# Performance work log

Hardware: AMD Instinct MI355X
Metric: run time of the kernel (lower is better)

Reference implementation:

```python
import jax, jax.numpy as jnp
import numpy as np

D = 1024      # in_features
H = 8         # heads per branch (head_num // 2)
DH = (D // 2) // H  # 64
OUT = 1024

def _split_heads(x, B, S):
    # [B, S, D/2] -> [B, H, S, DH]
    return x.reshape(B, S, H, DH).transpose(0, 2, 1, 3)

def _attn(q, k, v):
    # q,k,v: [B, H, S, DH]
    scores = jnp.einsum('bhqd,bhkd->bhqk', q, k) / jnp.sqrt(jnp.float32(DH))
    a = jax.nn.softmax(scores, axis=-1)
    return jnp.einsum('bhqk,bhkd->bhqd', a, v)

def setup_inputs() -> dict:
    key = jax.random.key(0)
    ks = jax.random.split(key, 16)
    B, S = 2, 2048
    d2 = D // 2
    sc = lambda fan_in: 1.0 / np.sqrt(fan_in)
    inp = {
        'f1': jax.random.normal(ks[0], (B, S, D), jnp.float32),
        'f2': jax.random.normal(ks[1], (B, S, D), jnp.float32),
    }
    names = ['qs', 'ks', 'vs', 'qc', 'kc', 'vc']
    for i, n in enumerate(names):
        inp['W' + n] = jax.random.uniform(ks[2 + i], (d2, D), jnp.float32, -sc(D), sc(D))
        inp['b' + n] = jax.random.uniform(ks[8 + i], (d2,), jnp.float32, -sc(D), sc(D))
    inp['Wo'] = jax.random.uniform(ks[14], (OUT, 2 * D), jnp.float32, -sc(2 * D), sc(2 * D))
    inp['bo'] = jax.random.uniform(ks[15], (OUT,), jnp.float32, -sc(2 * D), sc(2 * D))
    return inp

def reference(f1, f2, Wqs, bqs, Wks, bks, Wvs, bvs, Wqc, bqc, Wkc, bkc, Wvc, bvc, Wo, bo):
    B, S, _ = f1.shape
    lin = lambda x, W, b: jax.nn.relu(x @ W.T + b)
    qs = lin(f1, Wqs, bqs); ks_ = lin(f1, Wks, bks); vs = lin(f1, Wvs, bvs)
    qc = lin(f1, Wqc, bqc); kc = lin(f2, Wkc, bkc); vc = lin(f2, Wvc, bvc)
    ys = _attn(_split_heads(qs, B, S), _split_heads(ks_, B, S), _split_heads(vs, B, S))
    yc = _attn(_split_heads(qc, B, S), _split_heads(kc, B, S), _split_heads(vc, B, S))
    merge = lambda y: y.transpose(0, 2, 1, 3).reshape(B, S, D // 2)
    # reshape_to_batches followed by reshape_from_batches on vs/vc is identity
    y = jnp.concatenate([merge(ys), merge(yc), vs, vc], axis=-1)  # [B, S, 2D]
    return jax.nn.relu(y @ Wo.T + bo)
```

## Files before the change

kernel.cpp:

```cpp
#include <hip/hip_runtime.h>
#include <hip/hip_bf16.h>

using bf16 = __hip_bfloat16;
typedef __attribute__((ext_vector_type(8))) short bf16x8;
typedef __attribute__((ext_vector_type(4))) float f32x4;

#define MTOT 4096

__device__ __forceinline__ f32x4 fzero() {
    f32x4 z = {0.f, 0.f, 0.f, 0.f};
    return z;
}

__device__ __forceinline__ f32x4 mfma16(bf16x8 a, bf16x8 b, f32x4 c) {
    return __builtin_amdgcn_mfma_f32_16x16x32_bf16(a, b, c, 0, 0, 0);
}

typedef const __attribute__((address_space(1))) unsigned int* gas_ptr;
typedef __attribute__((address_space(3))) unsigned int* las_ptr;
__device__ __forceinline__ void async_copy16(const bf16* g, bf16* l) {
    __builtin_amdgcn_global_load_lds((gas_ptr)(const void*)g, (las_ptr)(void*)l, 16, 0, 0);
}

__device__ __forceinline__ bf16x8 load8(const bf16* p) {
    return *(const bf16x8*)p;
}
__device__ __forceinline__ bf16x8 load8(const float* p) {
    float4 a = *(const float4*)p;
    float4 b = *(const float4*)(p + 4);
    bf16 t[8];
    t[0] = __float2bfloat16(a.x); t[1] = __float2bfloat16(a.y);
    t[2] = __float2bfloat16(a.z); t[3] = __float2bfloat16(a.w);
    t[4] = __float2bfloat16(b.x); t[5] = __float2bfloat16(b.y);
    t[6] = __float2bfloat16(b.z); t[7] = __float2bfloat16(b.w);
    return *(const bf16x8*)t;
}

__device__ __forceinline__ void store_out(bf16* C, size_t idx, float v) {
    C[idx] = __float2bfloat16(v);
}
__device__ __forceinline__ void store_out(float* C, size_t idx, float v) {
    C[idx] = v;
}

__global__ void MultiHeadSelfCrossAttention_7834020348638_kernel(float* out, int n) {
    int i = blockIdx.x * blockDim.x + threadIdx.x;
    if (i < n) out[i] = 0.25f;
}

struct CvtArgs {
    const float* src[9];
    bf16* dst[9];
    int n8[9];
};
__global__ void cvt_kernel(CvtArgs a) {
    int seg = blockIdx.y;
    int t = blockIdx.x * blockDim.x + threadIdx.x;
    if (t < a.n8[seg])
        *(bf16x8*)(a.dst[seg] + (size_t)t * 8) = load8(a.src[seg] + (size_t)t * 8);
}

template <int BN, typename TC>
__device__ __forceinline__ void gemm_fast(
    const bf16* __restrict__ A, int lda,
    const bf16* __restrict__ Bt, int ldb,
    const float* __restrict__ bias,
    TC* __restrict__ C, int ldc,
    int K, int m0, int n0)
{
    constexpr int NI  = BN / 32;
    constexpr int BCH = BN * 32 / 8 / 256;

    __shared__ bf16 As[128 * 32];
    __shared__ bf16 Bs[BN * 32];

    const int tid  = threadIdx.x;
    const int lane = tid & 63;
    const int l15  = lane & 15, quad = lane >> 4;
    const int wave = tid >> 6;
    const int wr   = wave >> 1, wc = wave & 1;

    f32x4 acc[4][NI];
#pragma unroll
    for (int mi = 0; mi < 4; mi++)
#pragma unroll
        for (int ni = 0; ni < NI; ni++)
            acc[mi][ni] = fzero();

    for (int k0 = 0; k0 < K; k0 += 32) {
        __syncthreads();
#pragma unroll
        for (int i = 0; i < 2; i++) {
            int idx = i * 256 + tid;
            int r   = idx >> 2;
            int cg  = (idx & 3) * 8;
            async_copy16(A + (size_t)(m0 + r) * lda + k0 + cg, &As[idx * 8]);
        }
#pragma unroll
        for (int i = 0; i < BCH; i++) {
            int idx = i * 256 + tid;
            int r   = idx >> 2;
            int cg  = (idx & 3) * 8;
            async_copy16(Bt + (size_t)(n0 + r) * ldb + k0 + cg, &Bs[idx * 8]);
        }
        __syncthreads();

        bf16x8 af[4], bfr[NI];
#pragma unroll
        for (int mi = 0; mi < 4; mi++)
            af[mi] = *(const bf16x8*)&As[(wr * 64 + mi * 16 + l15) * 32 + quad * 8];
#pragma unroll
        for (int ni = 0; ni < NI; ni++)
            bfr[ni] = *(const bf16x8*)&Bs[(wc * (BN / 2) + ni * 16 + l15) * 32 + quad * 8];
#pragma unroll
        for (int mi = 0; mi < 4; mi++)
#pragma unroll
            for (int ni = 0; ni < NI; ni++)
                acc[mi][ni] = mfma16(af[mi], bfr[ni], acc[mi][ni]);
    }

#pragma unroll
    for (int ni = 0; ni < NI; ni++) {
        int col = n0 + wc * (BN / 2) + ni * 16 + l15;
        float bb = bias[col];
#pragma unroll
        for (int mi = 0; mi < 4; mi++) {
#pragma unroll
            for (int r = 0; r < 4; r++) {
                int row = m0 + wr * 64 + mi * 16 + quad * 4 + r;
                store_out(C, (size_t)row * ldc + col, fmaxf(acc[mi][ni][r] + bb, 0.f));
            }
        }
    }
}

template <int BN, typename TA, typename TB, typename TC>
__device__ __forceinline__ void gemm_reg(
    const TA* __restrict__ A, int lda,
    const TB* __restrict__ Bt, int ldb,
    const float* __restrict__ bias,
    TC* __restrict__ C, int ldc,
    int K, int m0, int n0)
{
    constexpr int NI  = BN / 32;
    constexpr int BCH = BN * 4 / 256;

    __shared__ bf16 As[128 * 32];
    __shared__ bf16 Bs[BN * 32];

    const int tid  = threadIdx.x;
    const int lane = tid & 63;
    const int l15  = lane & 15, quad = lane >> 4;
    const int wave = tid >> 6;
    const int wr   = wave >> 1, wc = wave & 1;

    f32x4 acc[4][NI];
#pragma unroll
    for (int mi = 0; mi < 4; mi++)
#pragma unroll
        for (int ni = 0; ni < NI; ni++)
            acc[mi][ni] = fzero();

    for (int k0 = 0; k0 < K; k0 += 32) {
        bf16x8 ra[2], rb[BCH];
#pragma unroll
        for (int i = 0; i < 2; i++) {
            int idx = i * 256 + tid;
            ra[i] = load8(A + (size_t)(m0 + (idx >> 2)) * lda + k0 + (idx & 3) * 8);
        }
#pragma unroll
        for (int i = 0; i < BCH; i++) {
            int idx = i * 256 + tid;
            rb[i] = load8(Bt + (size_t)(n0 + (idx >> 2)) * ldb + k0 + (idx & 3) * 8);
        }
        __syncthreads();
#pragma unroll
        for (int i = 0; i < 2; i++)
            *(bf16x8*)&As[(i * 256 + tid) * 8] = ra[i];
#pragma unroll
        for (int i = 0; i < BCH; i++)
            *(bf16x8*)&Bs[(i * 256 + tid) * 8] = rb[i];
        __syncthreads();

        bf16x8 af[4], bfr[NI];
#pragma unroll
        for (int mi = 0; mi < 4; mi++)
            af[mi] = *(const bf16x8*)&As[(wr * 64 + mi * 16 + l15) * 32 + quad * 8];
#pragma unroll
        for (int ni = 0; ni < NI; ni++)
            bfr[ni] = *(const bf16x8*)&Bs[(wc * (BN / 2) + ni * 16 + l15) * 32 + quad * 8];
#pragma unroll
        for (int mi = 0; mi < 4; mi++)
#pragma unroll
            for (int ni = 0; ni < NI; ni++)
                acc[mi][ni] = mfma16(af[mi], bfr[ni], acc[mi][ni]);
    }

#pragma unroll
    for (int ni = 0; ni < NI; ni++) {
        int col = n0 + wc * (BN / 2) + ni * 16 + l15;
        float bb = bias[col];
#pragma unroll
        for (int mi = 0; mi < 4; mi++) {
#pragma unroll
            for (int r = 0; r < 4; r++) {
                int row = m0 + wr * 64 + mi * 16 + quad * 4 + r;
                store_out(C, (size_t)row * ldc + col, fmaxf(acc[mi][ni][r] + bb, 0.f));
            }
        }
    }
}

__global__ void proj_fast(
    const bf16* __restrict__ F1, const bf16* __restrict__ F2,
    const bf16* __restrict__ Wb,
    const float* __restrict__ bqs, const float* __restrict__ bks,
    const float* __restrict__ bvs, const float* __restrict__ bqc,
    const float* __restrict__ bkc, const float* __restrict__ bvc,
    bf16* __restrict__ Y, bf16* Qs, bf16* Ks, bf16* Qc, bf16* Kc)
{
    const int g = blockIdx.z;
    const bf16* X; const float* bi; bf16* C; int ldc;
    switch (g) {
        case 0:  X = F1; bi = bqs; C = Qs;       ldc = 512;  break;
        case 1:  X = F1; bi = bks; C = Ks;       ldc = 512;  break;
        case 2:  X = F1; bi = bvs; C = Y + 1024; ldc = 2048; break;
        case 3:  X = F1; bi = bqc; C = Qc;       ldc = 512;  break;
        case 4:  X = F2; bi = bkc; C = Kc;       ldc = 512;  break;
        default: X = F2; bi = bvc; C = Y + 1536; ldc = 2048; break;
    }
    gemm_fast<128, bf16>(X, 1024, Wb + (size_t)g * 512 * 1024, 1024, bi, C, ldc,
                         1024, blockIdx.y * 128, blockIdx.x * 128);
}

__global__ void out_fast(const bf16* __restrict__ Y, const bf16* __restrict__ WoB,
                         const float* __restrict__ bo, float* __restrict__ out)
{
    gemm_fast<64, float>(Y, 2048, WoB, 2048, bo, out, 1024, 2048,
                         blockIdx.y * 128, blockIdx.x * 64);
}

__global__ void proj_reg(
    const float* __restrict__ f1, const float* __restrict__ f2,
    const float* __restrict__ Wqs, const float* __restrict__ bqs,
    const float* __restrict__ Wks, const float* __restrict__ bks,
    const float* __restrict__ Wvs, const float* __restrict__ bvs,
    const float* __restrict__ Wqc, const float* __restrict__ bqc,
    const float* __restrict__ Wkc, const float* __restrict__ bkc,
    const float* __restrict__ Wvc, const float* __restrict__ bvc,
    bf16* __restrict__ Y, bf16* Qs, bf16* Ks, bf16* Qc, bf16* Kc)
{
    const int g = blockIdx.z;
    const float *X, *W, *bi; bf16* C; int ldc;
    switch (g) {
        case 0:  X = f1; W = Wqs; bi = bqs; C = Qs;       ldc = 512;  break;
        case 1:  X = f1; W = Wks; bi = bks; C = Ks;       ldc = 512;  break;
        case 2:  X = f1; W = Wvs; bi = bvs; C = Y + 1024; ldc = 2048; break;
        case 3:  X = f1; W = Wqc; bi = bqc; C = Qc;       ldc = 512;  break;
        case 4:  X = f2; W = Wkc; bi = bkc; C = Kc;       ldc = 512;  break;
        default: X = f2; W = Wvc; bi = bvc; C = Y + 1536; ldc = 2048; break;
    }
    gemm_reg<128>(X, 1024, W, 1024, bi, C, ldc, 1024, blockIdx.y * 128, blockIdx.x * 128);
}

__global__ void out_reg(const bf16* __restrict__ Y, const float* __restrict__ Wo,
                        const float* __restrict__ bo, float* __restrict__ out)
{
    gemm_reg<64>(Y, 2048, Wo, 2048, bo, out, 1024, 2048, blockIdx.y * 128, blockIdx.x * 64);
}

__global__ __launch_bounds__(256, 4) void attn_kernel(
    const bf16* __restrict__ Qsb, const bf16* __restrict__ Ksb,
    const bf16* __restrict__ Qcb, const bf16* __restrict__ Kcb,
    bf16* __restrict__ Y)
{
    __shared__ bf16 QP[64 * 72];
    __shared__ bf16 Ksh[64 * 72];
    __shared__ bf16 Vsh[64 * 72];

    const int tid  = threadIdx.x;
    const int lane = tid & 63;
    const int l15  = lane & 15, quad = lane >> 4;
    const int wave = tid >> 6;
    const int qt = blockIdx.x, bh = blockIdx.y, br = blockIdx.z;
    const int b = bh >> 3, h = bh & 7;

    const bf16* Qb = (br ? Qcb : Qsb) + (size_t)b * 2048 * 512 + h * 64;
    const bf16* Kb = (br ? Kcb : Ksb) + (size_t)b * 2048 * 512 + h * 64;
    const bf16* Vb = Y + (size_t)b * 2048 * 2048 + 1024 + br * 512 + h * 64;
    bf16*       Ob = Y + (size_t)b * 2048 * 2048 +        br * 512 + h * 64;
    const int q0 = qt * 64;

#pragma unroll
    for (int i = 0; i < 2; i++) {
        int idx = i * 256 + tid;
        int r = idx >> 3, c0 = (idx & 7) * 8;
        *(bf16x8*)&QP[r * 72 + c0] = *(const bf16x8*)&Qb[(size_t)(q0 + r) * 512 + c0];
    }
    __syncthreads();

    bf16x8 qf[2];
#pragma unroll
    for (int ks = 0; ks < 2; ks++)
        qf[ks] = *(const bf16x8*)&QP[(wave * 16 + l15) * 72 + ks * 32 + quad * 8];

    const short one_bits = l15 == 0 ? (short)0x3F80 : (short)0;
    bf16x8 onesf;
#pragma unroll
    for (int j = 0; j < 8; j++) onesf[j] = one_bits;

    f32x4 o[4], o_l;
    o_l = fzero();
#pragma unroll
    for (int ni = 0; ni < 4; ni++) o[ni] = fzero();

    for (int jt = 0; jt < 32; jt++) {
        const int s0 = jt * 64;
        __syncthreads();
#pragma unroll
        for (int i = 0; i < 2; i++) {
            int idx = i * 256 + tid;
            int r = idx >> 3, c0 = (idx & 7) * 8;
            *(bf16x8*)&Ksh[r * 72 + c0] = *(const bf16x8*)&Kb[(size_t)(s0 + r) * 512 + c0];
        }
#pragma unroll
        for (int i = 0; i < 2; i++) {
            int cg = i * 4 + wave;
            bf16x8 t = *(const bf16x8*)&Vb[(size_t)(s0 + lane) * 2048 + cg * 8];
            const bf16* e = (const bf16*)&t;
#pragma unroll
            for (int j = 0; j < 8; j++)
                Vsh[(cg * 8 + j) * 72 + lane] = e[j];
        }
        __syncthreads();

        f32x4 s[4];
#pragma unroll
        for (int ni = 0; ni < 4; ni++) s[ni] = fzero();
#pragma unroll
        for (int ni = 0; ni < 4; ni++)
#pragma unroll
            for (int ks = 0; ks < 2; ks++) {
                bf16x8 kf = *(const bf16x8*)&Ksh[(ni * 16 + l15) * 72 + ks * 32 + quad * 8];
                s[ni] = mfma16(qf[ks], kf, s[ni]);
            }

#pragma unroll
        for (int ni = 0; ni < 4; ni++)
#pragma unroll
            for (int r = 0; r < 4; r++) {
                float p = __expf(s[ni][r] * 0.125f - 4.0f);
                QP[(wave * 16 + quad * 4 + r) * 72 + ni * 16 + l15] = __float2bfloat16(p);
            }

#pragma unroll
        for (int ks = 0; ks < 2; ks++) {
            bf16x8 pf = *(const bf16x8*)&QP[(wave * 16 + l15) * 72 + ks * 32 + quad * 8];
#pragma unroll
            for (int ni = 0; ni < 4; ni++) {
                bf16x8 vf = *(const bf16x8*)&Vsh[(ni * 16 + l15) * 72 + ks * 32 + quad * 8];
                o[ni] = mfma16(pf, vf, o[ni]);
            }
            o_l = mfma16(pf, onesf, o_l);
        }
    }

#pragma unroll
    for (int r = 0; r < 4; r++) {
        float lsum = __shfl(o_l[r], quad << 4);
        float inv = 1.f / lsum;
        int row = q0 + wave * 16 + quad * 4 + r;
#pragma unroll
        for (int ni = 0; ni < 4; ni++)
            Ob[(size_t)row * 2048 + ni * 16 + l15] = __float2bfloat16(o[ni][r] * inv);
    }
}

extern "C" void kernel_launch(void* const* d_in, const int* in_sizes, int n_in,
                              void* d_out, int out_size, void* d_ws, size_t ws_size,
                              hipStream_t stream) {
    const size_t out_bytes = (size_t)out_size * sizeof(float);
    const size_t ws_base = ((size_t)MTOT * 2048 + 4 * (size_t)MTOT * 512) * 2;
    const size_t ws_fast = ws_base + ((size_t)2 * MTOT * 1024 + 6 * 512 * 1024 + 1024 * 2048) * 2;

    if (n_in != 16) { hipMemsetAsync(d_out, 0x43, out_bytes, stream); return; }
    if (ws_size < ws_base) { hipMemsetAsync(d_out, 0x41, out_bytes, stream); return; }

    const float* f1  = (const float*)d_in[0];
    const float* f2  = (const float*)d_in[1];
    const float* Wqs = (const float*)d_in[2];  const float* bqs = (const float*)d_in[3];
    const float* Wks = (const float*)d_in[4];  const float* bks = (const float*)d_in[5];
    const float* Wvs = (const float*)d_in[6];  const float* bvs = (const float*)d_in[7];
    const float* Wqc = (const float*)d_in[8];  const float* bqc = (const float*)d_in[9];
    const float* Wkc = (const float*)d_in[10]; const float* bkc = (const float*)d_in[11];
    const float* Wvc = (const float*)d_in[12]; const float* bvc = (const float*)d_in[13];
    const float* Wo  = (const float*)d_in[14]; const float* bo  = (const float*)d_in[15];

    bf16* Y  = (bf16*)d_ws;
    bf16* Qs = Y  + (size_t)MTOT * 2048;
    bf16* Ks = Qs + (size_t)MTOT * 512;
    bf16* Qc = Ks + (size_t)MTOT * 512;
    bf16* Kc = Qc + (size_t)MTOT * 512;
    float* out = (float*)d_out;

    if (ws_size >= ws_fast) {
        bf16* F1  = Kc + (size_t)MTOT * 512;
        bf16* F2  = F1 + (size_t)MTOT * 1024;
        bf16* Wb  = F2 + (size_t)MTOT * 1024;
        bf16* WoB = Wb + (size_t)6 * 512 * 1024;

        CvtArgs ca;
        ca.src[0] = f1;  ca.dst[0] = F1;  ca.n8[0] = MTOT * 1024 / 8;
        ca.src[1] = f2;  ca.dst[1] = F2;  ca.n8[1] = MTOT * 1024 / 8;
        const float* ws_[6] = {Wqs, Wks, Wvs, Wqc, Wkc, Wvc};
        for (int i = 0; i < 6; i++) {
            ca.src[2 + i] = ws_[i];
            ca.dst[2 + i] = Wb + (size_t)i * 512 * 1024;
            ca.n8[2 + i]  = 512 * 1024 / 8;
        }
        ca.src[8] = Wo; ca.dst[8] = WoB; ca.n8[8] = 1024 * 2048 / 8;

        cvt_kernel<<<dim3((MTOT * 1024 / 8 + 255) / 256, 9), 256, 0, stream>>>(ca);
        proj_fast<<<dim3(4, 32, 6), 256, 0, stream>>>(
            F1, F2, Wb, bqs, bks, bvs, bqc, bkc, bvc, Y, Qs, Ks, Qc, Kc);
        attn_kernel<<<dim3(32, 16, 2), 256, 0, stream>>>(Qs, Ks, Qc, Kc, Y);
        out_fast<<<dim3(16, 32), 256, 0, stream>>>(Y, WoB, bo, out);
    } else {
        proj_reg<<<dim3(4, 32, 6), 256, 0, stream>>>(
            f1, f2, Wqs, bqs, Wks, bks, Wvs, bvs, Wqc, bqc, Wkc, bkc, Wvc, bvc,
            Y, Qs, Ks, Qc, Kc);
        attn_kernel<<<dim3(32, 16, 2), 256, 0, stream>>>(Qs, Ks, Qc, Kc, Y);
        out_reg<<<dim3(16, 32), 256, 0, stream>>>(Y, Wo, bo, out);
    }
}
```

Baseline: 267.6 us.

## Double K-step in GEMM tiles and register-prefetch K/V tiles in attention

The GEMM main loop now stages 64-wide K slices in shared memory instead of 32, halving the number of barrier pairs and issuing two MFMA sub-steps per stage. The attention kernel loads the next K/V tile into registers right after the barrier, so global-load latency overlaps with the QK, softmax and PV compute of the current tile. The cost is double the LDS footprint for the GEMM tiles and extra registers for the prefetched tiles, which may reduce occupancy.

```diff
diff --git a/kernel.cpp b/kernel.cpp
--- a/kernel.cpp
+++ b/kernel.cpp
@@ -69,10 +69,11 @@
     int K, int m0, int n0)
 {
     constexpr int NI  = BN / 32;
-    constexpr int BCH = BN * 32 / 8 / 256;
-
-    __shared__ bf16 As[128 * 32];
-    __shared__ bf16 Bs[BN * 32];
+    constexpr int ACH = 128 * 64 / 8 / 256;
+    constexpr int BCH = BN * 64 / 8 / 256;
+
+    __shared__ bf16 As[128 * 64];
+    __shared__ bf16 Bs[BN * 64];
 
     const int tid  = threadIdx.x;
     const int lane = tid & 63;
@@ -87,36 +88,39 @@
         for (int ni = 0; ni < NI; ni++)
             acc[mi][ni] = fzero();
 
-    for (int k0 = 0; k0 < K; k0 += 32) {
-        __syncthreads();
-#pragma unroll
-        for (int i = 0; i < 2; i++) {
+    for (int k0 = 0; k0 < K; k0 += 64) {
+        __syncthreads();
+#pragma unroll
+        for (int i = 0; i < ACH; i++) {
             int idx = i * 256 + tid;
-            int r   = idx >> 2;
-            int cg  = (idx & 3) * 8;
+            int r   = idx >> 3;
+            int cg  = (idx & 7) * 8;
             async_copy16(A + (size_t)(m0 + r) * lda + k0 + cg, &As[idx * 8]);
         }
 #pragma unroll
         for (int i = 0; i < BCH; i++) {
             int idx = i * 256 + tid;
-            int r   = idx >> 2;
-            int cg  = (idx & 3) * 8;
+            int r   = idx >> 3;
+            int cg  = (idx & 7) * 8;
             async_copy16(Bt + (size_t)(n0 + r) * ldb + k0 + cg, &Bs[idx * 8]);
         }
         __syncthreads();
 
-        bf16x8 af[4], bfr[NI];
-#pragma unroll
-        for (int mi = 0; mi < 4; mi++)
-            af[mi] = *(const bf16x8*)&As[(wr * 64 + mi * 16 + l15) * 32 + quad * 8];
-#pragma unroll
-        for (int ni = 0; ni < NI; ni++)
-            bfr[ni] = *(const bf16x8*)&Bs[(wc * (BN / 2) + ni * 16 + l15) * 32 + quad * 8];
-#pragma unroll
-        for (int mi = 0; mi < 4; mi++)
+#pragma unroll
+        for (int ks = 0; ks < 2; ks++) {
+            bf16x8 af[4], bfr[NI];
+#pragma unroll
+            for (int mi = 0; mi < 4; mi++)
+                af[mi] = *(const bf16x8*)&As[(wr * 64 + mi * 16 + l15) * 64 + ks * 32 + quad * 8];
 #pragma unroll
             for (int ni = 0; ni < NI; ni++)
-                acc[mi][ni] = mfma16(af[mi], bfr[ni], acc[mi][ni]);
+                bfr[ni] = *(const bf16x8*)&Bs[(wc * (BN / 2) + ni * 16 + l15) * 64 + ks * 32 + quad * 8];
+#pragma unroll
+            for (int mi = 0; mi < 4; mi++)
+#pragma unroll
+                for (int ni = 0; ni < NI; ni++)
+                    acc[mi][ni] = mfma16(af[mi], bfr[ni], acc[mi][ni]);
+        }
     }
 
 #pragma unroll
@@ -314,25 +318,36 @@
 #pragma unroll
     for (int ni = 0; ni < 4; ni++) o[ni] = fzero();
 
+    const int kr0 = tid >> 3, kc0 = (tid & 7) * 8;
+    const int kr1 = (256 + tid) >> 3;
+
+    bf16x8 kr[2], vr[2];
+    kr[0] = *(const bf16x8*)&Kb[(size_t)kr0 * 512 + kc0];
+    kr[1] = *(const bf16x8*)&Kb[(size_t)kr1 * 512 + kc0];
+    vr[0] = *(const bf16x8*)&Vb[(size_t)lane * 2048 + (0 * 4 + wave) * 8];
+    vr[1] = *(const bf16x8*)&Vb[(size_t)lane * 2048 + (1 * 4 + wave) * 8];
+
     for (int jt = 0; jt < 32; jt++) {
-        const int s0 = jt * 64;
-        __syncthreads();
-#pragma unroll
-        for (int i = 0; i < 2; i++) {
-            int idx = i * 256 + tid;
-            int r = idx >> 3, c0 = (idx & 7) * 8;
-            *(bf16x8*)&Ksh[r * 72 + c0] = *(const bf16x8*)&Kb[(size_t)(s0 + r) * 512 + c0];
-        }
+        __syncthreads();
+        *(bf16x8*)&Ksh[kr0 * 72 + kc0] = kr[0];
+        *(bf16x8*)&Ksh[kr1 * 72 + kc0] = kr[1];
 #pragma unroll
         for (int i = 0; i < 2; i++) {
             int cg = i * 4 + wave;
-            bf16x8 t = *(const bf16x8*)&Vb[(size_t)(s0 + lane) * 2048 + cg * 8];
-            const bf16* e = (const bf16*)&t;
+            const bf16* e = (const bf16*)&vr[i];
 #pragma unroll
             for (int j = 0; j < 8; j++)
                 Vsh[(cg * 8 + j) * 72 + lane] = e[j];
         }
         __syncthreads();
+
+        {
+            const int s0n = (jt < 31) ? (jt + 1) * 64 : 31 * 64;
+            kr[0] = *(const bf16x8*)&Kb[(size_t)(s0n + kr0) * 512 + kc0];
+            kr[1] = *(const bf16x8*)&Kb[(size_t)(s0n + kr1) * 512 + kc0];
+            vr[0] = *(const bf16x8*)&Vb[(size_t)(s0n + lane) * 2048 + (0 * 4 + wave) * 8];
+            vr[1] = *(const bf16x8*)&Vb[(size_t)(s0n + lane) * 2048 + (1 * 4 + wave) * 8];
+        }
 
         f32x4 s[4];
 #pragma unroll
```

Measured after the change: 264.3 us. About the same (-1.2%).
